# Performance work log

Hardware: AMD Instinct MI355X
Metric: run time of the kernel (lower is better)

## Reference

```python
import jax, jax.numpy as jnp
import numpy as np

N = 100_000      # nodes
E = 3_200_000    # edges (avg degree 32)
F_IN = 64        # num_node_features
G = 256          # graphs in batch


def _lin(key, fan_in, fan_out):
    kw, kb = jax.random.split(key)
    bound = 1.0 / np.sqrt(fan_in)
    W = jax.random.uniform(kw, (fan_in, fan_out), jnp.float32, -bound, bound)
    b = jax.random.uniform(kb, (fan_out,), jnp.float32, -bound, bound)
    return W, b


def setup_inputs() -> dict:
    key = jax.random.key(0)
    ks = jax.random.split(key, 9)
    x = jax.random.normal(ks[0], (N, F_IN), jnp.float32)
    edge_index = jax.random.randint(ks[1], (2, E), 0, N, dtype=jnp.int64)
    batch = jnp.sort(jax.random.randint(ks[2], (N,), 0, G, dtype=jnp.int64))
    W1, b1 = _lin(ks[3], F_IN, 60)
    W2, b2 = _lin(ks[4], 60, 50)
    Wf1, bf1 = _lin(ks[5], 50, 30)
    Wf2, bf2 = _lin(ks[6], 30, 20)
    Wf3, bf3 = _lin(ks[7], 20, 10)
    Wo, bo = _lin(ks[8], 10, 1)
    return {"x": x, "edge_index": edge_index, "batch": batch,
            "W1": W1, "b1": b1, "W2": W2, "b2": b2,
            "Wf1": Wf1, "bf1": bf1, "Wf2": Wf2, "bf2": bf2,
            "Wf3": Wf3, "bf3": bf3, "Wo": Wo, "bo": bo}


def _gcn_norm(edge_index, n_nodes):
    # add self loops, then symmetric D^{-1/2} (A+I) D^{-1/2} edge weights
    loop = jnp.arange(n_nodes, dtype=edge_index.dtype)
    src = jnp.concatenate([edge_index[0], loop])
    dst = jnp.concatenate([edge_index[1], loop])
    deg = jax.ops.segment_sum(jnp.ones_like(dst, dtype=jnp.float32), dst,
                              num_segments=n_nodes)
    dinv = jax.lax.rsqrt(deg)  # deg >= 1 thanks to self loops
    norm = dinv[src] * dinv[dst]
    return src, dst, norm


def _gcn_conv(h, W, b, src, dst, norm, n_nodes):
    h = h @ W                                            # [N, out]
    msg = h[src] * norm[:, None]                         # gather over edges
    agg = jax.ops.segment_sum(msg, dst, num_segments=n_nodes)
    return agg + b


def reference(x, edge_index, batch, W1, b1, W2, b2,
              Wf1, bf1, Wf2, bf2, Wf3, bf3, Wo, bo):
    n_nodes = x.shape[0]
    src, dst, norm = _gcn_norm(edge_index, n_nodes)
    h = _gcn_conv(x, W1, b1, src, dst, norm, n_nodes)    # [N, 60]
    h = _gcn_conv(h, W2, b2, src, dst, norm, n_nodes)    # [N, 50]
    # global_add_pool over graph ids
    g = jax.ops.segment_sum(h, batch, num_segments=G)    # [G, 50]
    # MLP stack (no nonlinearities in the original forward)
    g = g @ Wf1 + bf1
    g = g @ Wf2 + bf2
    g = g @ Wf3 + bf3
    return g @ Wo + bo                                   # [G, 1]
```

## Files before the change

### kernel.cpp

```cpp
#include <hip/hip_runtime.h>


#define RSHIFT 7
#define RNODES 128
#define MAXNB  1024
#define BINBLOCKS 192
#define BINTHREADS 512

__global__ void collapse_weights_k(
    const float* __restrict__ W1, const float* __restrict__ b1,
    const float* __restrict__ W2, const float* __restrict__ b2,
    const float* __restrict__ Wf1, const float* __restrict__ bf1,
    const float* __restrict__ Wf2, const float* __restrict__ bf2,
    const float* __restrict__ Wf3, const float* __restrict__ bf3,
    const float* __restrict__ Wo, const float* __restrict__ bo,
    float* __restrict__ w1c, float* __restrict__ sc,
    int* __restrict__ cnt, int nb)
{
    __shared__ float wo[10], w3[20], w2[30], w1[50], w2c[60];
    const int t = threadIdx.x;
    for (int b = t; b < nb; b += 64) cnt[b] = 0;
    if (t < 10) wo[t] = Wo[t];
    __syncthreads();
    if (t < 20) { float s = 0.f; for (int j = 0; j < 10; ++j) s += Wf3[t*10+j]*wo[j]; w3[t] = s; }
    __syncthreads();
    if (t < 30) { float s = 0.f; for (int j = 0; j < 20; ++j) s += Wf2[t*20+j]*w3[j]; w2[t] = s; }
    __syncthreads();
    if (t < 50) { float s = 0.f; for (int j = 0; j < 30; ++j) s += Wf1[t*30+j]*w2[j]; w1[t] = s; }
    __syncthreads();
    if (t < 60) { float s = 0.f; for (int j = 0; j < 50; ++j) s += W2[t*50+j]*w1[j]; w2c[t] = s; }
    __syncthreads();
    { float s = 0.f; for (int j = 0; j < 60; ++j) s += W1[t*60+j]*w2c[j]; w1c[t] = s; }
    if (t == 0) {
        float c1 = 0.f; for (int j = 0; j < 60; ++j) c1 += b1[j]*w2c[j];
        float c2 = 0.f; for (int j = 0; j < 50; ++j) c2 += b2[j]*w1[j];
        float c0 = bo[0];
        for (int j = 0; j < 30; ++j) c0 += bf1[j]*w2[j];
        for (int j = 0; j < 20; ++j) c0 += bf2[j]*w3[j];
        for (int j = 0; j < 10; ++j) c0 += bf3[j]*wo[j];
        sc[0] = c1; sc[1] = c2; sc[2] = c0;
    }
}

__global__ void node_u_k(const float* __restrict__ x, const float* __restrict__ w1c,
                         float* __restrict__ u, int n) {
    int tid = blockIdx.x * blockDim.x + threadIdx.x;
    int wave = tid >> 6;
    int lane = threadIdx.x & 63;
    int node = wave * 4 + (lane >> 4);
    int sub = lane & 15;
    if (node >= n) return;
    float4 xv = *reinterpret_cast<const float4*>(x + (size_t)node * 64 + sub * 4);
    float4 wv = *reinterpret_cast<const float4*>(w1c + sub * 4);
    float val = xv.x * wv.x + xv.y * wv.y + xv.z * wv.z + xv.w * wv.w;
    val += __shfl_down(val, 8, 16);
    val += __shfl_down(val, 4, 16);
    val += __shfl_down(val, 2, 16);
    val += __shfl_down(val, 1, 16);
    if (sub == 0) u[node] = val;
}

__global__ void bin_count_k(const int* __restrict__ dst, int E, int chunk,
                            int nb, int* __restrict__ cnt) {
    __shared__ int hist[MAXNB];
    int e0 = blockIdx.x * chunk;
    int e1 = e0 + chunk; if (e1 > E) e1 = E;
    if (e0 >= E) return;
    for (int b = threadIdx.x; b < nb; b += blockDim.x) hist[b] = 0;
    __syncthreads();
    for (int i = e0 + (int)threadIdx.x * 4; i + 3 < e1; i += blockDim.x * 4) {
        int4 d = *reinterpret_cast<const int4*>(dst + i);
        atomicAdd(&hist[d.x >> RSHIFT], 1);
        atomicAdd(&hist[d.y >> RSHIFT], 1);
        atomicAdd(&hist[d.z >> RSHIFT], 1);
        atomicAdd(&hist[d.w >> RSHIFT], 1);
    }
    int rem = (e1 - e0) & 3;
    if ((int)threadIdx.x < rem) atomicAdd(&hist[dst[e1 - rem + threadIdx.x] >> RSHIFT], 1);
    __syncthreads();
    for (int b = threadIdx.x; b < nb; b += blockDim.x)
        if (hist[b]) atomicAdd(&cnt[b], hist[b]);
}

__global__ void scan_init_k(const int* __restrict__ cnt, int nb,
                            int* __restrict__ base, int* __restrict__ cursor,
                            const float* __restrict__ sc, float* __restrict__ out, int G) {
    __shared__ int sums[256];
    int t = threadIdx.x;
    if (t < G) out[t] = sc[2];
    int v[4]; int s = 0;
    #pragma unroll
    for (int j = 0; j < 4; ++j) {
        int b = t * 4 + j;
        v[j] = (b < nb) ? ((cnt[b] + 3) & ~3) : 0;
        s += v[j];
    }
    sums[t] = s;
    __syncthreads();
    for (int off = 1; off < 256; off <<= 1) {
        int xv = (t >= off) ? sums[t - off] : 0;
        __syncthreads();
        sums[t] += xv;
        __syncthreads();
    }
    int run = sums[t] - s;
    #pragma unroll
    for (int j = 0; j < 4; ++j) {
        int b = t * 4 + j;
        if (b < nb) { base[b] = run; cursor[b] = run; }
        run += v[j];
    }
}

__global__ void bin_scatter_k(const int* __restrict__ src, const int* __restrict__ dst,
                              int E, int chunk, int nb,
                              int* __restrict__ cursor, unsigned int* __restrict__ binned) {
    __shared__ int hist[MAXNB];
    int e0 = blockIdx.x * chunk;
    int e1 = e0 + chunk; if (e1 > E) e1 = E;
    if (e0 >= E) return;
    for (int b = threadIdx.x; b < nb; b += blockDim.x) hist[b] = 0;
    __syncthreads();
    for (int i = e0 + (int)threadIdx.x * 4; i + 3 < e1; i += blockDim.x * 4) {
        int4 d = *reinterpret_cast<const int4*>(dst + i);
        atomicAdd(&hist[d.x >> RSHIFT], 1);
        atomicAdd(&hist[d.y >> RSHIFT], 1);
        atomicAdd(&hist[d.z >> RSHIFT], 1);
        atomicAdd(&hist[d.w >> RSHIFT], 1);
    }
    int rem = (e1 - e0) & 3;
    if ((int)threadIdx.x < rem) atomicAdd(&hist[dst[e1 - rem + threadIdx.x] >> RSHIFT], 1);
    __syncthreads();
    for (int b = threadIdx.x; b < nb; b += blockDim.x) {
        int c = hist[b];
        hist[b] = c ? atomicAdd(&cursor[b], c) : 0;
    }
    __syncthreads();
    for (int i = e0 + (int)threadIdx.x * 4; i + 3 < e1; i += blockDim.x * 4) {
        int4 s4 = *reinterpret_cast<const int4*>(src + i);
        int4 d4 = *reinterpret_cast<const int4*>(dst + i);
        int p;
        p = atomicAdd(&hist[d4.x >> RSHIFT], 1);
        binned[p] = (unsigned)s4.x | ((unsigned)(d4.x & (RNODES-1)) << 17);
        p = atomicAdd(&hist[d4.y >> RSHIFT], 1);
        binned[p] = (unsigned)s4.y | ((unsigned)(d4.y & (RNODES-1)) << 17);
        p = atomicAdd(&hist[d4.z >> RSHIFT], 1);
        binned[p] = (unsigned)s4.z | ((unsigned)(d4.z & (RNODES-1)) << 17);
        p = atomicAdd(&hist[d4.w >> RSHIFT], 1);
        binned[p] = (unsigned)s4.w | ((unsigned)(d4.w & (RNODES-1)) << 17);
    }
    if ((int)threadIdx.x < rem) {
        int i = e1 - rem + threadIdx.x;
        int s = src[i], d = dst[i];
        int p = atomicAdd(&hist[d >> RSHIFT], 1);
        binned[p] = (unsigned)s | ((unsigned)(d & (RNODES-1)) << 17);
    }
}

__global__ void degree_k(const unsigned int* __restrict__ binned, const int* __restrict__ base,
                         const int* __restrict__ endp, const float* __restrict__ u,
                         float* __restrict__ dinv, float* __restrict__ w, int n) {
    __shared__ int cnt[RNODES];
    int tid = threadIdx.x, b = blockIdx.x;
    if (tid < RNODES) cnt[tid] = 0;
    __syncthreads();
    int s0 = base[b], s1 = endp[b];
    int nvec = (s1 - s0) >> 2;
    for (int k = tid; k < nvec; k += blockDim.x) {
        uint4 p = *reinterpret_cast<const uint4*>(binned + s0 + 4 * k);
        atomicAdd(&cnt[p.x >> 17], 1);
        atomicAdd(&cnt[p.y >> 17], 1);
        atomicAdd(&cnt[p.z >> 17], 1);
        atomicAdd(&cnt[p.w >> 17], 1);
    }
    int i = s0 + 4 * nvec + tid;
    if (i < s1) atomicAdd(&cnt[binned[i] >> 17], 1);
    __syncthreads();
    int g = (b << RSHIFT) + tid;
    if (tid < RNODES && g < n) {
        float d = rsqrtf((float)(cnt[tid] + 1));
        dinv[g] = d;
        w[g] = d * u[g];
    }
}

__global__ void conv_mid_k(const unsigned int* __restrict__ binned, const int* __restrict__ base,
                           const int* __restrict__ endp,
                           const float* __restrict__ w, const float* __restrict__ dinv,
                           const float* __restrict__ u, const float* __restrict__ sc,
                           float* __restrict__ v, float* __restrict__ wb, int n) {
    __shared__ float acc[RNODES];
    int tid = threadIdx.x, b = blockIdx.x;
    if (tid < RNODES) acc[tid] = 0.f;
    __syncthreads();
    int s0 = base[b], s1 = endp[b];
    int nvec = (s1 - s0) >> 2;
    for (int k = tid; k < nvec; k += blockDim.x) {
        uint4 p = *reinterpret_cast<const uint4*>(binned + s0 + 4 * k);
        float wx = w[p.x & 0x1FFFF];
        float wy = w[p.y & 0x1FFFF];
        float wz = w[p.z & 0x1FFFF];
        float ww = w[p.w & 0x1FFFF];
        atomicAdd(&acc[p.x >> 17], wx);
        atomicAdd(&acc[p.y >> 17], wy);
        atomicAdd(&acc[p.z >> 17], wz);
        atomicAdd(&acc[p.w >> 17], ww);
    }
    int i = s0 + 4 * nvec + tid;
    if (i < s1) { unsigned p = binned[i]; atomicAdd(&acc[p >> 17], w[p & 0x1FFFF]); }
    __syncthreads();
    int g = (b << RSHIFT) + tid;
    if (tid < RNODES && g < n) {
        float di = dinv[g];
        float val = sc[0] + di * acc[tid] + di * di * u[g];
        v[g] = val;
        wb[g] = di * val;
    }
}

__global__ void conv_final_k(const unsigned int* __restrict__ binned, const int* __restrict__ base,
                             const int* __restrict__ endp,
                             const float* __restrict__ wb, const float* __restrict__ dinv,
                             const float* __restrict__ v, const float* __restrict__ sc,
                             const int* __restrict__ batch, float* __restrict__ out, int n) {
    __shared__ float acc[RNODES];
    __shared__ float tbuf[RNODES];
    __shared__ int gbuf[RNODES];
    int tid = threadIdx.x, b = blockIdx.x;
    if (tid < RNODES) acc[tid] = 0.f;
    __syncthreads();
    int s0 = base[b], s1 = endp[b];
    int nvec = (s1 - s0) >> 2;
    for (int k = tid; k < nvec; k += blockDim.x) {
        uint4 p = *reinterpret_cast<const uint4*>(binned + s0 + 4 * k);
        float wx = wb[p.x & 0x1FFFF];
        float wy = wb[p.y & 0x1FFFF];
        float wz = wb[p.z & 0x1FFFF];
        float ww = wb[p.w & 0x1FFFF];
        atomicAdd(&acc[p.x >> 17], wx);
        atomicAdd(&acc[p.y >> 17], wy);
        atomicAdd(&acc[p.z >> 17], wz);
        atomicAdd(&acc[p.w >> 17], ww);
    }
    int i = s0 + 4 * nvec + tid;
    if (i < s1) { unsigned p = binned[i]; atomicAdd(&acc[p >> 17], wb[p & 0x1FFFF]); }
    __syncthreads();
    int g = (b << RSHIFT) + tid;
    float tval = 0.f; int gid = -1;
    if (tid < RNODES && g < n) {
        float di = dinv[g];
        tval = sc[1] + di * acc[tid] + di * di * v[g];
        gid = batch[g];
    }
    if (tid < RNODES) { tbuf[tid] = tval; gbuf[tid] = gid; }
    __syncthreads();
    if (tid < RNODES && g < n) {
        bool head = (tid == 0) || (gbuf[tid - 1] != gid);
        if (head) {
            float s = 0.f;
            int i2 = tid;
            while (i2 < RNODES && gbuf[i2] == gid) { s += tbuf[i2]; ++i2; }
            atomicAdd(&out[gid], s);
        }
    }
}

extern "C" void kernel_launch(void* const* d_in, const int* in_sizes, int n_in,
                              void* d_out, int out_size, void* d_ws, size_t ws_size,
                              hipStream_t stream)
{
    const float* x    = (const float*)d_in[0];
    const int*   ei   = (const int*)d_in[1];
    const int*   batch= (const int*)d_in[2];
    const float* W1   = (const float*)d_in[3];
    const float* b1   = (const float*)d_in[4];
    const float* W2   = (const float*)d_in[5];
    const float* b2   = (const float*)d_in[6];
    const float* Wf1  = (const float*)d_in[7];
    const float* bf1  = (const float*)d_in[8];
    const float* Wf2  = (const float*)d_in[9];
    const float* bf2  = (const float*)d_in[10];
    const float* Wf3  = (const float*)d_in[11];
    const float* bf3  = (const float*)d_in[12];
    const float* Wo   = (const float*)d_in[13];
    const float* bo   = (const float*)d_in[14];
    float* out = (float*)d_out;

    const int n = in_sizes[0] / 64;
    const int E = in_sizes[1] / 2;
    const int G = out_size;
    const int* src = ei;
    const int* dst = ei + E;
    const int nb = (n + RNODES - 1) >> RSHIFT;

    float* ws_f = (float*)d_ws;
    int*   ws_i = (int*)d_ws;
    float* w1c   = ws_f;
    float* sc    = ws_f + 64;
    int*   cnt   = ws_i + 128;
    int*   basep = ws_i + 1280;
    int*   cursor= ws_i + 2432;
    float* u     = ws_f + 3584;
    float* dinv  = u + n;
    float* w     = dinv + n;
    float* v     = w + n;
    float* wb    = v + n;
    unsigned int* binned = (unsigned int*)(wb + n);

    int chunk = (E + BINBLOCKS - 1) / BINBLOCKS;
    chunk = (chunk + 3) & ~3;

    hipLaunchKernelGGL(collapse_weights_k, dim3(1), dim3(64), 0, stream,
                       W1, b1, W2, b2, Wf1, bf1, Wf2, bf2, Wf3, bf3, Wo, bo,
                       w1c, sc, cnt, nb);
    hipLaunchKernelGGL(node_u_k, dim3((n / 4 * 64 + 255) / 256 + 1), dim3(256), 0, stream,
                       x, w1c, u, n);
    hipLaunchKernelGGL(bin_count_k, dim3(BINBLOCKS), dim3(BINTHREADS), 0, stream,
                       dst, E, chunk, nb, cnt);
    hipLaunchKernelGGL(scan_init_k, dim3(1), dim3(256), 0, stream,
                       cnt, nb, basep, cursor, sc, out, G);
    hipLaunchKernelGGL(bin_scatter_k, dim3(BINBLOCKS), dim3(BINTHREADS), 0, stream,
                       src, dst, E, chunk, nb, cursor, binned);
    hipLaunchKernelGGL(degree_k, dim3(nb), dim3(256), 0, stream,
                       binned, basep, cursor, u, dinv, w, n);
    hipLaunchKernelGGL(conv_mid_k, dim3(nb), dim3(256), 0, stream,
                       binned, basep, cursor, w, dinv, u, sc, v, wb, n);
    hipLaunchKernelGGL(conv_final_k, dim3(nb), dim3(256), 0, stream,
                       binned, basep, cursor, wb, dinv, v, sc, batch, out, n);
}
```

Measured before the change: 222.0 us.

## Make edge binning deterministic with per-block offsets and LDS-staged coalesced scatter

Replaces the global atomic cursor counting sort with a per-block histogram matrix, a two-level scan (per-bin across blocks, then across bins), and a scatter that stages each block's packed edges in LDS sorted by bin before writing them contiguously to global memory. This is meant to remove global atomics and scattered 4-byte writes in favour of mostly coalesced stores. The block count rises to 512, and the later per-bin kernels now launch with 512 threads. The trade-offs are extra kernel launches, a large LDS footprint per block that limits occupancy, and reuse of the binned buffer as scratch for the count matrix.

```diff
diff --git a/kernel.cpp b/kernel.cpp
--- a/kernel.cpp
+++ b/kernel.cpp
@@ -3,9 +3,10 @@
 
 #define RSHIFT 7
 #define RNODES 128
-#define MAXNB  1024
-#define BINBLOCKS 192
-#define BINTHREADS 512
+#define NB_MAX 1024
+#define NBLK 512
+#define STHREADS 512
+#define STAGE_CAP 8192
 
 __global__ void collapse_weights_k(
     const float* __restrict__ W1, const float* __restrict__ b1,
@@ -14,12 +15,10 @@
     const float* __restrict__ Wf2, const float* __restrict__ bf2,
     const float* __restrict__ Wf3, const float* __restrict__ bf3,
     const float* __restrict__ Wo, const float* __restrict__ bo,
-    float* __restrict__ w1c, float* __restrict__ sc,
-    int* __restrict__ cnt, int nb)
+    float* __restrict__ w1c, float* __restrict__ sc)
 {
     __shared__ float wo[10], w3[20], w2[30], w1[50], w2c[60];
     const int t = threadIdx.x;
-    for (int b = t; b < nb; b += 64) cnt[b] = 0;
     if (t < 10) wo[t] = Wo[t];
     __syncthreads();
     if (t < 20) { float s = 0.f; for (int j = 0; j < 10; ++j) s += Wf3[t*10+j]*wo[j]; w3[t] = s; }
@@ -61,99 +60,149 @@
 }
 
 __global__ void bin_count_k(const int* __restrict__ dst, int E, int chunk,
-                            int nb, int* __restrict__ cnt) {
-    __shared__ int hist[MAXNB];
+                            int nb, int* __restrict__ cnt_bm) {
+    __shared__ int hist[NB_MAX];
+    int tid = threadIdx.x;
+    hist[tid] = 0; hist[tid + 512] = 0;
+    __syncthreads();
     int e0 = blockIdx.x * chunk;
     int e1 = e0 + chunk; if (e1 > E) e1 = E;
-    if (e0 >= E) return;
-    for (int b = threadIdx.x; b < nb; b += blockDim.x) hist[b] = 0;
-    __syncthreads();
-    for (int i = e0 + (int)threadIdx.x * 4; i + 3 < e1; i += blockDim.x * 4) {
-        int4 d = *reinterpret_cast<const int4*>(dst + i);
-        atomicAdd(&hist[d.x >> RSHIFT], 1);
-        atomicAdd(&hist[d.y >> RSHIFT], 1);
-        atomicAdd(&hist[d.z >> RSHIFT], 1);
-        atomicAdd(&hist[d.w >> RSHIFT], 1);
-    }
-    int rem = (e1 - e0) & 3;
-    if ((int)threadIdx.x < rem) atomicAdd(&hist[dst[e1 - rem + threadIdx.x] >> RSHIFT], 1);
-    __syncthreads();
-    for (int b = threadIdx.x; b < nb; b += blockDim.x)
-        if (hist[b]) atomicAdd(&cnt[b], hist[b]);
-}
-
-__global__ void scan_init_k(const int* __restrict__ cnt, int nb,
-                            int* __restrict__ base, int* __restrict__ cursor,
-                            const float* __restrict__ sc, float* __restrict__ out, int G) {
-    __shared__ int sums[256];
+    for (int j = 0; j < STAGE_CAP / (STHREADS * 4); ++j) {
+        int i = e0 + tid * 4 + j * (STHREADS * 4);
+        if (i + 3 < e1) {
+            int4 d = *reinterpret_cast<const int4*>(dst + i);
+            atomicAdd(&hist[d.x >> RSHIFT], 1);
+            atomicAdd(&hist[d.y >> RSHIFT], 1);
+            atomicAdd(&hist[d.z >> RSHIFT], 1);
+            atomicAdd(&hist[d.w >> RSHIFT], 1);
+        } else if (i < e1) {
+            for (int k = i; k < e1; ++k) atomicAdd(&hist[dst[k] >> RSHIFT], 1);
+        }
+    }
+    __syncthreads();
+    for (int b = tid; b < nb; b += STHREADS)
+        cnt_bm[(size_t)blockIdx.x * nb + b] = hist[b];
+}
+
+__global__ void scanA_k(const int* __restrict__ cnt_bm, int nb,
+                        int* __restrict__ offs, int* __restrict__ total) {
+    __shared__ int sums[STHREADS];
+    int k = threadIdx.x, b = blockIdx.x;
+    int v = cnt_bm[(size_t)k * nb + b];
+    sums[k] = v;
+    __syncthreads();
+    for (int off = 1; off < STHREADS; off <<= 1) {
+        int a = (k >= off) ? sums[k - off] : 0;
+        __syncthreads();
+        sums[k] += a;
+        __syncthreads();
+    }
+    offs[(size_t)b * NBLK + k] = sums[k] - v;
+    if (k == STHREADS - 1) total[b] = sums[k];
+}
+
+__global__ void scanB_k(const int* __restrict__ total, int nb,
+                        int* __restrict__ base, int* __restrict__ endp,
+                        const float* __restrict__ sc, float* __restrict__ out, int G) {
+    __shared__ int sums[STHREADS];
     int t = threadIdx.x;
     if (t < G) out[t] = sc[2];
-    int v[4]; int s = 0;
-    #pragma unroll
-    for (int j = 0; j < 4; ++j) {
-        int b = t * 4 + j;
-        v[j] = (b < nb) ? ((cnt[b] + 3) & ~3) : 0;
-        s += v[j];
-    }
-    sums[t] = s;
-    __syncthreads();
-    for (int off = 1; off < 256; off <<= 1) {
-        int xv = (t >= off) ? sums[t - off] : 0;
-        __syncthreads();
-        sums[t] += xv;
-        __syncthreads();
-    }
-    int run = sums[t] - s;
-    #pragma unroll
-    for (int j = 0; j < 4; ++j) {
-        int b = t * 4 + j;
-        if (b < nb) { base[b] = run; cursor[b] = run; }
-        run += v[j];
-    }
+    int b0 = 2 * t, b1 = 2 * t + 1;
+    int t0 = (b0 < nb) ? total[b0] : 0;
+    int t1 = (b1 < nb) ? total[b1] : 0;
+    int a0 = (t0 + 3) & ~3, a1 = (t1 + 3) & ~3;
+    int pair = a0 + a1;
+    sums[t] = pair;
+    __syncthreads();
+    for (int off = 1; off < STHREADS; off <<= 1) {
+        int a = (t >= off) ? sums[t - off] : 0;
+        __syncthreads();
+        sums[t] += a;
+        __syncthreads();
+    }
+    int excl = sums[t] - pair;
+    if (b0 < nb) { base[b0] = excl; endp[b0] = excl + t0; }
+    if (b1 < nb) { base[b1] = excl + a0; endp[b1] = excl + a0 + t1; }
 }
 
 __global__ void bin_scatter_k(const int* __restrict__ src, const int* __restrict__ dst,
                               int E, int chunk, int nb,
-                              int* __restrict__ cursor, unsigned int* __restrict__ binned) {
-    __shared__ int hist[MAXNB];
+                              const int* __restrict__ base, const int* __restrict__ offs,
+                              unsigned int* __restrict__ binned) {
+    __shared__ int hist[NB_MAX];
+    __shared__ int tbase[NB_MAX];
+    __shared__ int adj[NB_MAX];
+    __shared__ int sums[STHREADS];
+    __shared__ unsigned int staged[STAGE_CAP];
+    __shared__ unsigned short bof[STAGE_CAP];
+    const int tid = threadIdx.x;
+    hist[tid] = 0; hist[tid + 512] = 0;
+    __syncthreads();
     int e0 = blockIdx.x * chunk;
     int e1 = e0 + chunk; if (e1 > E) e1 = E;
-    if (e0 >= E) return;
-    for (int b = threadIdx.x; b < nb; b += blockDim.x) hist[b] = 0;
-    __syncthreads();
-    for (int i = e0 + (int)threadIdx.x * 4; i + 3 < e1; i += blockDim.x * 4) {
-        int4 d = *reinterpret_cast<const int4*>(dst + i);
-        atomicAdd(&hist[d.x >> RSHIFT], 1);
-        atomicAdd(&hist[d.y >> RSHIFT], 1);
-        atomicAdd(&hist[d.z >> RSHIFT], 1);
-        atomicAdd(&hist[d.w >> RSHIFT], 1);
-    }
-    int rem = (e1 - e0) & 3;
-    if ((int)threadIdx.x < rem) atomicAdd(&hist[dst[e1 - rem + threadIdx.x] >> RSHIFT], 1);
-    __syncthreads();
-    for (int b = threadIdx.x; b < nb; b += blockDim.x) {
-        int c = hist[b];
-        hist[b] = c ? atomicAdd(&cursor[b], c) : 0;
-    }
-    __syncthreads();
-    for (int i = e0 + (int)threadIdx.x * 4; i + 3 < e1; i += blockDim.x * 4) {
-        int4 s4 = *reinterpret_cast<const int4*>(src + i);
-        int4 d4 = *reinterpret_cast<const int4*>(dst + i);
-        int p;
-        p = atomicAdd(&hist[d4.x >> RSHIFT], 1);
-        binned[p] = (unsigned)s4.x | ((unsigned)(d4.x & (RNODES-1)) << 17);
-        p = atomicAdd(&hist[d4.y >> RSHIFT], 1);
-        binned[p] = (unsigned)s4.y | ((unsigned)(d4.y & (RNODES-1)) << 17);
-        p = atomicAdd(&hist[d4.z >> RSHIFT], 1);
-        binned[p] = (unsigned)s4.z | ((unsigned)(d4.z & (RNODES-1)) << 17);
-        p = atomicAdd(&hist[d4.w >> RSHIFT], 1);
-        binned[p] = (unsigned)s4.w | ((unsigned)(d4.w & (RNODES-1)) << 17);
-    }
-    if ((int)threadIdx.x < rem) {
-        int i = e1 - rem + threadIdx.x;
-        int s = src[i], d = dst[i];
-        int p = atomicAdd(&hist[d >> RSHIFT], 1);
-        binned[p] = (unsigned)s | ((unsigned)(d & (RNODES-1)) << 17);
+    const int QMAX = STAGE_CAP / (STHREADS * 4);
+    unsigned int pk[QMAX * 4];
+    int bk[QMAX * 4];
+    int rk[QMAX * 4];
+    int nv[QMAX];
+    #pragma unroll
+    for (int j = 0; j < QMAX; ++j) {
+        int i = e0 + tid * 4 + j * (STHREADS * 4);
+        int cnt = e1 - i; if (cnt > 4) cnt = 4; if (cnt < 0) cnt = 0;
+        nv[j] = cnt;
+        if (cnt == 4) {
+            int4 s4 = *reinterpret_cast<const int4*>(src + i);
+            int4 d4 = *reinterpret_cast<const int4*>(dst + i);
+            pk[j*4+0] = (unsigned)s4.x | ((unsigned)(d4.x & (RNODES-1)) << 17);
+            pk[j*4+1] = (unsigned)s4.y | ((unsigned)(d4.y & (RNODES-1)) << 17);
+            pk[j*4+2] = (unsigned)s4.z | ((unsigned)(d4.z & (RNODES-1)) << 17);
+            pk[j*4+3] = (unsigned)s4.w | ((unsigned)(d4.w & (RNODES-1)) << 17);
+            bk[j*4+0] = d4.x >> RSHIFT; bk[j*4+1] = d4.y >> RSHIFT;
+            bk[j*4+2] = d4.z >> RSHIFT; bk[j*4+3] = d4.w >> RSHIFT;
+            rk[j*4+0] = atomicAdd(&hist[bk[j*4+0]], 1);
+            rk[j*4+1] = atomicAdd(&hist[bk[j*4+1]], 1);
+            rk[j*4+2] = atomicAdd(&hist[bk[j*4+2]], 1);
+            rk[j*4+3] = atomicAdd(&hist[bk[j*4+3]], 1);
+        } else {
+            for (int l = 0; l < cnt; ++l) {
+                int s = src[i + l], d = dst[i + l];
+                pk[j*4+l] = (unsigned)s | ((unsigned)(d & (RNODES-1)) << 17);
+                bk[j*4+l] = d >> RSHIFT;
+                rk[j*4+l] = atomicAdd(&hist[bk[j*4+l]], 1);
+            }
+        }
+    }
+    __syncthreads();
+    int h0 = hist[2*tid], h1 = hist[2*tid+1];
+    int pair = h0 + h1;
+    sums[tid] = pair;
+    __syncthreads();
+    for (int off = 1; off < STHREADS; off <<= 1) {
+        int a = (tid >= off) ? sums[tid - off] : 0;
+        __syncthreads();
+        sums[tid] += a;
+        __syncthreads();
+    }
+    int excl = sums[tid] - pair;
+    tbase[2*tid] = excl;
+    tbase[2*tid+1] = excl + h0;
+    for (int b = 2*tid; b <= 2*tid+1; ++b)
+        if (b < nb) adj[b] = base[b] + offs[(size_t)b * NBLK + blockIdx.x] - tbase[b];
+    __syncthreads();
+    #pragma unroll
+    for (int j = 0; j < QMAX; ++j) {
+        for (int l = 0; l < nv[j]; ++l) {
+            int b = bk[j*4+l];
+            int slot = tbase[b] + rk[j*4+l];
+            staged[slot] = pk[j*4+l];
+            bof[slot] = (unsigned short)b;
+        }
+    }
+    __syncthreads();
+    int tcount = e1 - e0;
+    for (int s = tid; s < tcount; s += STHREADS) {
+        int b = bof[s];
+        binned[adj[b] + s] = staged[s];
     }
 }
 
@@ -295,36 +344,43 @@
 
     float* ws_f = (float*)d_ws;
     int*   ws_i = (int*)d_ws;
-    float* w1c   = ws_f;
-    float* sc    = ws_f + 64;
-    int*   cnt   = ws_i + 128;
-    int*   basep = ws_i + 1280;
-    int*   cursor= ws_i + 2432;
-    float* u     = ws_f + 3584;
-    float* dinv  = u + n;
-    float* w     = dinv + n;
-    float* v     = w + n;
-    float* wb    = v + n;
-    unsigned int* binned = (unsigned int*)(wb + n);
-
-    int chunk = (E + BINBLOCKS - 1) / BINBLOCKS;
+    float* w1c    = ws_f;
+    float* sc     = ws_f + 64;
+    int*   basep  = ws_i + 128;
+    int*   endp   = ws_i + 128 + NB_MAX;
+    int*   total  = ws_i + 128 + 2*NB_MAX;
+    int*   offs   = ws_i + 128 + 3*NB_MAX;
+    size_t off_u  = 128 + 3*(size_t)NB_MAX + (size_t)nb * NBLK;
+    off_u = (off_u + 3) & ~(size_t)3;
+    float* u      = ws_f + off_u;
+    float* dinv   = u + n;
+    float* w      = dinv + n;
+    float* v      = w + n;
+    float* wb     = v + n;
+    size_t off_b  = off_u + 5*(size_t)n;
+    off_b = (off_b + 3) & ~(size_t)3;
+    unsigned int* binned = (unsigned int*)(ws_f + off_b);
+    int* cnt_bm = (int*)binned;
+
+    int chunk = (E + NBLK - 1) / NBLK;
     chunk = (chunk + 3) & ~3;
 
     hipLaunchKernelGGL(collapse_weights_k, dim3(1), dim3(64), 0, stream,
-                       W1, b1, W2, b2, Wf1, bf1, Wf2, bf2, Wf3, bf3, Wo, bo,
-                       w1c, sc, cnt, nb);
+                       W1, b1, W2, b2, Wf1, bf1, Wf2, bf2, Wf3, bf3, Wo, bo, w1c, sc);
     hipLaunchKernelGGL(node_u_k, dim3((n / 4 * 64 + 255) / 256 + 1), dim3(256), 0, stream,
                        x, w1c, u, n);
-    hipLaunchKernelGGL(bin_count_k, dim3(BINBLOCKS), dim3(BINTHREADS), 0, stream,
-                       dst, E, chunk, nb, cnt);
-    hipLaunchKernelGGL(scan_init_k, dim3(1), dim3(256), 0, stream,
-                       cnt, nb, basep, cursor, sc, out, G);
-    hipLaunchKernelGGL(bin_scatter_k, dim3(BINBLOCKS), dim3(BINTHREADS), 0, stream,
-                       src, dst, E, chunk, nb, cursor, binned);
-    hipLaunchKernelGGL(degree_k, dim3(nb), dim3(256), 0, stream,
-                       binned, basep, cursor, u, dinv, w, n);
-    hipLaunchKernelGGL(conv_mid_k, dim3(nb), dim3(256), 0, stream,
-                       binned, basep, cursor, w, dinv, u, sc, v, wb, n);
-    hipLaunchKernelGGL(conv_final_k, dim3(nb), dim3(256), 0, stream,
-                       binned, basep, cursor, wb, dinv, v, sc, batch, out, n);
-}
+    hipLaunchKernelGGL(bin_count_k, dim3(NBLK), dim3(STHREADS), 0, stream,
+                       dst, E, chunk, nb, cnt_bm);
+    hipLaunchKernelGGL(scanA_k, dim3(nb), dim3(STHREADS), 0, stream,
+                       cnt_bm, nb, offs, total);
+    hipLaunchKernelGGL(scanB_k, dim3(1), dim3(STHREADS), 0, stream,
+                       total, nb, basep, endp, sc, out, G);
+    hipLaunchKernelGGL(bin_scatter_k, dim3(NBLK), dim3(STHREADS), 0, stream,
+                       src, dst, E, chunk, nb, basep, offs, binned);
+    hipLaunchKernelGGL(degree_k, dim3(nb), dim3(512), 0, stream,
+                       binned, basep, endp, u, dinv, w, n);
+    hipLaunchKernelGGL(conv_mid_k, dim3(nb), dim3(512), 0, stream,
+                       binned, basep, endp, w, dinv, u, sc, v, wb, n);
+    hipLaunchKernelGGL(conv_final_k, dim3(nb), dim3(512), 0, stream,
+                       binned, basep, endp, wb, dinv, v, sc, batch, out, n);
+}
```

Result: faster. 204.0 us (-8.1%).
